# Kernel tuning notes

Hardware: AMD Instinct MI355X
Metric: run time of the kernel (lower is better)

The kernel has to match this reference:

```python
import jax, jax.numpy as jnp
import numpy as np

BATCH, S, N_DIM, B_SIZE = 512, 66, 304, 128

def setup_inputs() -> dict:
    key = jax.random.key(0)
    kx, kw = jax.random.split(key)
    x = jax.random.normal(kx, (BATCH, S, N_DIM), dtype=jnp.float32)
    W = jax.random.normal(kw, (B_SIZE, N_DIM), dtype=jnp.float32) * (1.0 / np.sqrt(N_DIM))
    b = jnp.zeros((B_SIZE,), dtype=jnp.float32)
    return {"x": x, "W": W, "b": b}

def reference(x, W, b):
    # Linear projection into tree space: (batch, S, B_size)
    t = jnp.einsum('bsd,kd->bsk', x, W) + b
    # Pairwise squared distances over sentence positions, same math as
    # expand/transpose/subtract/pow(2)/sum in the torch module.
    diff = t[:, :, None, :] - t[:, None, :, :]        # (batch, S, S, B_size)
    return jnp.sum(diff * diff, axis=-1)               # (batch, S, S)
```

## Files before the change

kernel.cpp:

```cpp
#include <hip/hip_runtime.h>
#include <hip/hip_bf16.h>

#define NBATCH 512
#define NS 66
#define ND 304
#define NK 128

#define XROWS 80
#define XSTRIDE_B 640
#define XBYTES (XROWS * XSTRIDE_B)
#define TSTRIDE_B 256
#define TBYTES (XROWS * TSTRIDE_B)
#define GSTRIDE 84

#define NTHREADS 512

typedef __attribute__((ext_vector_type(8))) short bf16x8;
typedef __attribute__((ext_vector_type(4))) short s16x4;
typedef __attribute__((ext_vector_type(4))) float f32x4;

__device__ __forceinline__ short f2bf(float x) {
    return __builtin_bit_cast(short, __float2bfloat16(x));
}

__global__ __launch_bounds__(NTHREADS, 4) void treeprobe_mfma(
    const float* __restrict__ x,
    const float* __restrict__ W,
    float* __restrict__ out)
{
    __shared__ __align__(16) char lds[XBYTES + TBYTES];
    char* const t_lds = lds + XBYTES;
    float* const G = (float*)lds;

    const int tid   = threadIdx.x;
    const int batch = blockIdx.x;
    const int lane  = tid & 63;
    const int wv    = tid >> 6;
    const int lr    = lane & 15;
    const int lg    = lane >> 4;

    bf16x8 wfrag[10];
    {
        const int c = wv * 16 + lr;
        const float* __restrict__ wr = W + c * ND;
#pragma unroll
        for (int kk = 0; kk < 10; ++kk) {
            const int k0 = kk * 32 + lg * 8;
            bf16x8 f = {0, 0, 0, 0, 0, 0, 0, 0};
            if (k0 < ND) {
                const float4 p0 = *reinterpret_cast<const float4*>(wr + k0);
                const float4 p1 = *reinterpret_cast<const float4*>(wr + k0 + 4);
                f[0] = f2bf(p0.x); f[1] = f2bf(p0.y);
                f[2] = f2bf(p0.z); f[3] = f2bf(p0.w);
                f[4] = f2bf(p1.x); f[5] = f2bf(p1.y);
                f[6] = f2bf(p1.z); f[7] = f2bf(p1.w);
            }
            wfrag[kk] = f;
        }
    }

    for (int i = tid; i < XBYTES / 16; i += NTHREADS) {
        *reinterpret_cast<f32x4*>(lds + i * 16) = (f32x4){0.f, 0.f, 0.f, 0.f};
    }
    __syncthreads();

    const float* __restrict__ xb = x + (size_t)batch * NS * ND;
    for (int e = tid; e < NS * ND / 4; e += NTHREADS) {
        const int s  = e / 76;
        const int d4 = (e % 76) * 4;
        const float4 v = *reinterpret_cast<const float4*>(xb + e * 4);
        int byte = s * XSTRIDE_B + d4 * 2;
        byte ^= (s & 7) << 4;
        s16x4 sv;
        sv[0] = f2bf(v.x); sv[1] = f2bf(v.y);
        sv[2] = f2bf(v.z); sv[3] = f2bf(v.w);
        *reinterpret_cast<s16x4*>(lds + byte) = sv;
    }
    __syncthreads();

    f32x4 acc[5];
#pragma unroll
    for (int mt = 0; mt < 5; ++mt) acc[mt] = (f32x4){0.f, 0.f, 0.f, 0.f};

#pragma unroll
    for (int kk = 0; kk < 10; ++kk) {
        bf16x8 a[5];
#pragma unroll
        for (int mt = 0; mt < 5; ++mt) {
            const int row = mt * 16 + lr;
            int byte = row * XSTRIDE_B + kk * 64 + lg * 16;
            byte ^= (row & 7) << 4;
            a[mt] = *reinterpret_cast<const bf16x8*>(lds + byte);
        }
#pragma unroll
        for (int mt = 0; mt < 5; ++mt)
            acc[mt] = __builtin_amdgcn_mfma_f32_16x16x32_bf16(
                a[mt], wfrag[kk], acc[mt], 0, 0, 0);
    }

    {
        const int col = wv * 16 + lr;
#pragma unroll
        for (int mt = 0; mt < 5; ++mt) {
#pragma unroll
            for (int r = 0; r < 4; ++r) {
                const int row = mt * 16 + lg * 4 + r;
                int byte = row * TSTRIDE_B + col * 2;
                byte ^= (row & 7) << 4;
                *reinterpret_cast<short*>(t_lds + byte) = f2bf(acc[mt][r]);
            }
        }
    }
    __syncthreads();

    for (int tile = wv; tile < 25; tile += 8) {
        const int ti = tile / 5, tj = tile % 5;
        f32x4 g = (f32x4){0.f, 0.f, 0.f, 0.f};
#pragma unroll
        for (int kk = 0; kk < 4; ++kk) {
            const int ra = ti * 16 + lr;
            int ba = ra * TSTRIDE_B + kk * 64 + lg * 16;
            ba ^= (ra & 7) << 4;
            const int rb = tj * 16 + lr;
            int bb = rb * TSTRIDE_B + kk * 64 + lg * 16;
            bb ^= (rb & 7) << 4;
            const bf16x8 av = *reinterpret_cast<const bf16x8*>(t_lds + ba);
            const bf16x8 bv = *reinterpret_cast<const bf16x8*>(t_lds + bb);
            g = __builtin_amdgcn_mfma_f32_16x16x32_bf16(av, bv, g, 0, 0, 0);
        }
#pragma unroll
        for (int r = 0; r < 4; ++r) {
            const int row = ti * 16 + lg * 4 + r;
            const int col = tj * 16 + lr;
            G[row * GSTRIDE + col] = g[r];
        }
    }
    __syncthreads();

    float* __restrict__ ob = out + (size_t)batch * NS * NS;
    for (int e = tid; e < NS * NS / 2; e += NTHREADS) {
        const int i = e / 33;
        const int j = (e % 33) * 2;
        const float nii = G[i * GSTRIDE + i];
        float2 r;
        r.x = nii + G[j * GSTRIDE + j] - 2.f * G[i * GSTRIDE + j];
        r.y = nii + G[(j + 1) * GSTRIDE + (j + 1)] - 2.f * G[i * GSTRIDE + j + 1];
        *reinterpret_cast<float2*>(ob + i * NS + j) = r;
    }
}

extern "C" void kernel_launch(void* const* d_in, const int* in_sizes, int n_in,
                              void* d_out, int out_size, void* d_ws, size_t ws_size,
                              hipStream_t stream) {
    const float* x = (const float*)d_in[0];
    const float* W = (const float*)d_in[1];
    float* out = (float*)d_out;

    treeprobe_mfma<<<NBATCH, NTHREADS, 0, stream>>>(x, W, out);
}
```

Measured before the change: 21.26 us.

## Split x load into two halves overlapped with MFMA and exploit Gram symmetry

The x tile is loaded into registers in two column halves, so the second half's global loads are in flight while the first half's MFMAs run, and only the padding regions are zeroed instead of the whole buffer. The projection MFMA swaps its operands so each lane holds four contiguous output columns and writes t with vector stores. The Gram step computes only the 15 upper-triangular tiles, reads norms from the diagonal tiles, and writes distances straight from registers to global memory for both (i,j) and (j,i). This removes the G scratch buffer and an extra barrier/pass, at the cost of more registers and scattered, uncoalesced transposed global stores.

```diff
diff --git a/kernel.cpp b/kernel.cpp
--- a/kernel.cpp
+++ b/kernel.cpp
@@ -11,8 +11,6 @@
 #define XBYTES (XROWS * XSTRIDE_B)
 #define TSTRIDE_B 256
 #define TBYTES (XROWS * TSTRIDE_B)
-#define GSTRIDE 84
-
 #define NTHREADS 512
 
 typedef __attribute__((ext_vector_type(8))) short bf16x8;
@@ -22,15 +20,18 @@
 __device__ __forceinline__ short f2bf(float x) {
     return __builtin_bit_cast(short, __float2bfloat16(x));
 }
+
+__device__ const int TI_LUT[15] = {0,1,2,3,4, 0,0,0,0,1,1,1,2,2,3};
+__device__ const int TJ_LUT[15] = {0,1,2,3,4, 1,2,3,4,2,3,4,3,4,4};
 
 __global__ __launch_bounds__(NTHREADS, 4) void treeprobe_mfma(
     const float* __restrict__ x,
     const float* __restrict__ W,
     float* __restrict__ out)
 {
-    __shared__ __align__(16) char lds[XBYTES + TBYTES];
+    __shared__ __align__(16) char lds[XBYTES + TBYTES + 80 * 4];
     char* const t_lds = lds + XBYTES;
-    float* const G = (float*)lds;
+    float* const norms = (float*)(lds + XBYTES + TBYTES);
 
     const int tid   = threadIdx.x;
     const int batch = blockIdx.x;
@@ -38,6 +39,28 @@
     const int wv    = tid >> 6;
     const int lr    = lane & 15;
     const int lg    = lane >> 4;
+
+    const float* __restrict__ xb = x + (size_t)batch * NS * ND;
+
+    float4 aA[6];
+#pragma unroll
+    for (int i = 0; i < 6; ++i) {
+        const int e = tid + i * NTHREADS;
+        aA[i] = (e < 2640)
+            ? *reinterpret_cast<const float4*>(xb + (e / 40) * ND + (e % 40) * 4)
+            : make_float4(0.f, 0.f, 0.f, 0.f);
+    }
+
+    for (int i = tid; i < 560; i += NTHREADS) {
+        const int row = 66 + i / 40;
+        *reinterpret_cast<f32x4*>(lds + row * XSTRIDE_B + (i % 40) * 16) =
+            (f32x4){0.f, 0.f, 0.f, 0.f};
+    }
+    for (int i = tid; i < 132; i += NTHREADS) {
+        const int row = i >> 1;
+        const int byte = (row * XSTRIDE_B + 608 + (i & 1) * 16) ^ ((row & 7) << 4);
+        *reinterpret_cast<f32x4*>(lds + byte) = (f32x4){0.f, 0.f, 0.f, 0.f};
+    }
 
     bf16x8 wfrag[10];
     {
@@ -59,93 +82,166 @@
         }
     }
 
-    for (int i = tid; i < XBYTES / 16; i += NTHREADS) {
-        *reinterpret_cast<f32x4*>(lds + i * 16) = (f32x4){0.f, 0.f, 0.f, 0.f};
-    }
-    __syncthreads();
-
-    const float* __restrict__ xb = x + (size_t)batch * NS * ND;
-    for (int e = tid; e < NS * ND / 4; e += NTHREADS) {
-        const int s  = e / 76;
-        const int d4 = (e % 76) * 4;
-        const float4 v = *reinterpret_cast<const float4*>(xb + e * 4);
-        int byte = s * XSTRIDE_B + d4 * 2;
-        byte ^= (s & 7) << 4;
+#pragma unroll
+    for (int i = 0; i < 6; ++i) {
+        const int e = tid + i * NTHREADS;
+        if (e < 2640) {
+            const int s = e / 40;
+            const int f = (e % 40) * 4;
+            const int byte = (s * XSTRIDE_B + f * 2) ^ ((s & 7) << 4);
+            s16x4 sv;
+            sv[0] = f2bf(aA[i].x); sv[1] = f2bf(aA[i].y);
+            sv[2] = f2bf(aA[i].z); sv[3] = f2bf(aA[i].w);
+            *reinterpret_cast<s16x4*>(lds + byte) = sv;
+        }
+    }
+
+    float4 aB[5];
+#pragma unroll
+    for (int i = 0; i < 5; ++i) {
+        const int e = tid + i * NTHREADS;
+        aB[i] = (e < 2376)
+            ? *reinterpret_cast<const float4*>(xb + (e / 36) * ND + 160 + (e % 36) * 4)
+            : make_float4(0.f, 0.f, 0.f, 0.f);
+    }
+    __syncthreads();
+
+    f32x4 acc[5];
+#pragma unroll
+    for (int st = 0; st < 5; ++st) acc[st] = (f32x4){0.f, 0.f, 0.f, 0.f};
+
+#pragma unroll
+    for (int kk = 0; kk < 5; ++kk) {
+        bf16x8 a[5];
+#pragma unroll
+        for (int st = 0; st < 5; ++st) {
+            const int row = st * 16 + lr;
+            const int byte = (row * XSTRIDE_B + kk * 64 + lg * 16) ^ ((row & 7) << 4);
+            a[st] = *reinterpret_cast<const bf16x8*>(lds + byte);
+        }
+#pragma unroll
+        for (int st = 0; st < 5; ++st)
+            acc[st] = __builtin_amdgcn_mfma_f32_16x16x32_bf16(
+                wfrag[kk], a[st], acc[st], 0, 0, 0);
+    }
+
+#pragma unroll
+    for (int i = 0; i < 5; ++i) {
+        const int e = tid + i * NTHREADS;
+        if (e < 2376) {
+            const int s = e / 36;
+            const int f = 160 + (e % 36) * 4;
+            const int byte = (s * XSTRIDE_B + f * 2) ^ ((s & 7) << 4);
+            s16x4 sv;
+            sv[0] = f2bf(aB[i].x); sv[1] = f2bf(aB[i].y);
+            sv[2] = f2bf(aB[i].z); sv[3] = f2bf(aB[i].w);
+            *reinterpret_cast<s16x4*>(lds + byte) = sv;
+        }
+    }
+    __syncthreads();
+
+#pragma unroll
+    for (int kk = 5; kk < 10; ++kk) {
+        bf16x8 a[5];
+#pragma unroll
+        for (int st = 0; st < 5; ++st) {
+            const int row = st * 16 + lr;
+            const int byte = (row * XSTRIDE_B + kk * 64 + lg * 16) ^ ((row & 7) << 4);
+            a[st] = *reinterpret_cast<const bf16x8*>(lds + byte);
+        }
+#pragma unroll
+        for (int st = 0; st < 5; ++st)
+            acc[st] = __builtin_amdgcn_mfma_f32_16x16x32_bf16(
+                wfrag[kk], a[st], acc[st], 0, 0, 0);
+    }
+
+#pragma unroll
+    for (int st = 0; st < 5; ++st) {
+        const int s = st * 16 + lr;
+        const int c0 = wv * 16 + lg * 4;
+        const int byte = (s * TSTRIDE_B + c0 * 2) ^ ((s & 7) << 4);
         s16x4 sv;
-        sv[0] = f2bf(v.x); sv[1] = f2bf(v.y);
-        sv[2] = f2bf(v.z); sv[3] = f2bf(v.w);
-        *reinterpret_cast<s16x4*>(lds + byte) = sv;
-    }
-    __syncthreads();
-
-    f32x4 acc[5];
-#pragma unroll
-    for (int mt = 0; mt < 5; ++mt) acc[mt] = (f32x4){0.f, 0.f, 0.f, 0.f};
-
-#pragma unroll
-    for (int kk = 0; kk < 10; ++kk) {
-        bf16x8 a[5];
-#pragma unroll
-        for (int mt = 0; mt < 5; ++mt) {
-            const int row = mt * 16 + lr;
-            int byte = row * XSTRIDE_B + kk * 64 + lg * 16;
-            byte ^= (row & 7) << 4;
-            a[mt] = *reinterpret_cast<const bf16x8*>(lds + byte);
-        }
-#pragma unroll
-        for (int mt = 0; mt < 5; ++mt)
-            acc[mt] = __builtin_amdgcn_mfma_f32_16x16x32_bf16(
-                a[mt], wfrag[kk], acc[mt], 0, 0, 0);
-    }
+        sv[0] = f2bf(acc[st][0]); sv[1] = f2bf(acc[st][1]);
+        sv[2] = f2bf(acc[st][2]); sv[3] = f2bf(acc[st][3]);
+        *reinterpret_cast<s16x4*>(t_lds + byte) = sv;
+    }
+    __syncthreads();
+
+    const int idx0 = wv;
+    const int idx1 = wv + 8;
+    const int ti0 = TI_LUT[idx0], tj0 = TJ_LUT[idx0];
+
+    f32x4 g0 = (f32x4){0.f, 0.f, 0.f, 0.f};
+#pragma unroll
+    for (int kk = 0; kk < 4; ++kk) {
+        const int ra = ti0 * 16 + lr;
+        const int ba = (ra * TSTRIDE_B + kk * 64 + lg * 16) ^ ((ra & 7) << 4);
+        const int rb = tj0 * 16 + lr;
+        const int bb = (rb * TSTRIDE_B + kk * 64 + lg * 16) ^ ((rb & 7) << 4);
+        g0 = __builtin_amdgcn_mfma_f32_16x16x32_bf16(
+            *reinterpret_cast<const bf16x8*>(t_lds + ba),
+            *reinterpret_cast<const bf16x8*>(t_lds + bb), g0, 0, 0, 0);
+    }
+    if (wv < 5) {
+#pragma unroll
+        for (int r = 0; r < 4; ++r)
+            if (lr == lg * 4 + r) norms[wv * 16 + lr] = g0[r];
+    }
+
+    f32x4 g1 = (f32x4){0.f, 0.f, 0.f, 0.f};
+    int ti1 = 0, tj1 = 0;
+    if (idx1 < 15) {
+        ti1 = TI_LUT[idx1]; tj1 = TJ_LUT[idx1];
+#pragma unroll
+        for (int kk = 0; kk < 4; ++kk) {
+            const int ra = ti1 * 16 + lr;
+            const int ba = (ra * TSTRIDE_B + kk * 64 + lg * 16) ^ ((ra & 7) << 4);
+            const int rb = tj1 * 16 + lr;
+            const int bb = (rb * TSTRIDE_B + kk * 64 + lg * 16) ^ ((rb & 7) << 4);
+            g1 = __builtin_amdgcn_mfma_f32_16x16x32_bf16(
+                *reinterpret_cast<const bf16x8*>(t_lds + ba),
+                *reinterpret_cast<const bf16x8*>(t_lds + bb), g1, 0, 0, 0);
+        }
+    }
+    __syncthreads();
+
+    float* __restrict__ ob = out + (size_t)batch * NS * NS;
 
     {
-        const int col = wv * 16 + lr;
-#pragma unroll
-        for (int mt = 0; mt < 5; ++mt) {
+        const int j = tj0 * 16 + lr;
+        const float nj = norms[j];
+        float v[4];
+#pragma unroll
+        for (int r = 0; r < 4; ++r) {
+            const int i = ti0 * 16 + lg * 4 + r;
+            v[r] = norms[i] + nj - 2.f * g0[r];
+            if (i < NS && j < NS) ob[i * NS + j] = v[r];
+        }
+        if (ti0 != tj0 && j < NS) {
 #pragma unroll
             for (int r = 0; r < 4; ++r) {
-                const int row = mt * 16 + lg * 4 + r;
-                int byte = row * TSTRIDE_B + col * 2;
-                byte ^= (row & 7) << 4;
-                *reinterpret_cast<short*>(t_lds + byte) = f2bf(acc[mt][r]);
+                const int i = ti0 * 16 + lg * 4 + r;
+                if (i < NS) ob[j * NS + i] = v[r];
             }
         }
     }
-    __syncthreads();
-
-    for (int tile = wv; tile < 25; tile += 8) {
-        const int ti = tile / 5, tj = tile % 5;
-        f32x4 g = (f32x4){0.f, 0.f, 0.f, 0.f};
-#pragma unroll
-        for (int kk = 0; kk < 4; ++kk) {
-            const int ra = ti * 16 + lr;
-            int ba = ra * TSTRIDE_B + kk * 64 + lg * 16;
-            ba ^= (ra & 7) << 4;
-            const int rb = tj * 16 + lr;
-            int bb = rb * TSTRIDE_B + kk * 64 + lg * 16;
-            bb ^= (rb & 7) << 4;
-            const bf16x8 av = *reinterpret_cast<const bf16x8*>(t_lds + ba);
-            const bf16x8 bv = *reinterpret_cast<const bf16x8*>(t_lds + bb);
-            g = __builtin_amdgcn_mfma_f32_16x16x32_bf16(av, bv, g, 0, 0, 0);
-        }
+    if (idx1 < 15) {
+        const int j = tj1 * 16 + lr;
+        const float nj = norms[j];
+        float v[4];
 #pragma unroll
         for (int r = 0; r < 4; ++r) {
-            const int row = ti * 16 + lg * 4 + r;
-            const int col = tj * 16 + lr;
-            G[row * GSTRIDE + col] = g[r];
-        }
-    }
-    __syncthreads();
-
-    float* __restrict__ ob = out + (size_t)batch * NS * NS;
-    for (int e = tid; e < NS * NS / 2; e += NTHREADS) {
-        const int i = e / 33;
-        const int j = (e % 33) * 2;
-        const float nii = G[i * GSTRIDE + i];
-        float2 r;
-        r.x = nii + G[j * GSTRIDE + j] - 2.f * G[i * GSTRIDE + j];
-        r.y = nii + G[(j + 1) * GSTRIDE + (j + 1)] - 2.f * G[i * GSTRIDE + j + 1];
-        *reinterpret_cast<float2*>(ob + i * NS + j) = r;
+            const int i = ti1 * 16 + lg * 4 + r;
+            v[r] = norms[i] + nj - 2.f * g1[r];
+            if (i < NS && j < NS) ob[i * NS + j] = v[r];
+        }
+        if (j < NS) {
+#pragma unroll
+            for (int r = 0; r < 4; ++r) {
+                const int i = ti1 * 16 + lg * 4 + r;
+                if (i < NS) ob[j * NS + i] = v[r];
+            }
+        }
     }
 }
 
```

Result: faster. 20.82 us (-2.1%).
